# Performance work log

Hardware: AMD Instinct MI355X
Metric: run time of the kernel (lower is better)

## Reference

```python
import jax, jax.numpy as jnp
import numpy as np

N_NODES = 50000
N_EDGES = 500000
NFEAT = 128
NHID = 128
NOUT = 16


def setup_inputs() -> dict:
    key = jax.random.key(0)
    ks = jax.random.split(key, 8)
    x = jax.random.normal(ks[0], (N_NODES, NFEAT), dtype=jnp.float32)
    edge_src = jax.random.randint(ks[1], (N_EDGES,), 0, N_NODES, dtype=jnp.int32)
    edge_dst = jax.random.randint(ks[2], (N_EDGES,), 0, N_NODES, dtype=jnp.int32)
    edge_weight = jax.random.uniform(ks[3], (N_EDGES,), dtype=jnp.float32)
    # Glorot-ish init for linear weights, zero bias (PyG GCNConv default bias=0)
    def glorot(k, fan_in, fan_out):
        s = jnp.sqrt(6.0 / (fan_in + fan_out))
        return jax.random.uniform(k, (fan_in, fan_out), jnp.float32, -s, s)
    W1 = glorot(ks[4], NFEAT, NHID)
    W2 = glorot(ks[5], NHID, NHID)
    W3 = glorot(ks[6], NHID, NOUT)
    b1 = jnp.zeros((NHID,), jnp.float32)
    b2 = jnp.zeros((NHID,), jnp.float32)
    b3 = jnp.zeros((NOUT,), jnp.float32)
    return {"x": x, "edge_src": edge_src, "edge_dst": edge_dst,
            "edge_weight": edge_weight, "W1": W1, "b1": b1,
            "W2": W2, "b2": b2, "W3": W3, "b3": b3}


def gcn_conv(x, src, dst, ew, W, b):
    """PyG GCNConv: symmetric-normalized aggregation with self-loops (weight 1).

    out_i = sum_{(j->i)} d_i^{-1/2} w_ji d_j^{-1/2} (x_j W) + d_i^{-1} (x_i W) + b
    where d_i = 1 + sum of incoming edge weights.
    """
    n = x.shape[0]
    xw = x @ W                                            # [N, F_out]
    deg = jax.ops.segment_sum(ew, dst, num_segments=n) + 1.0  # self-loop weight 1
    dinv = jnp.where(deg > 0, jax.lax.rsqrt(deg), 0.0)    # d^{-1/2}
    norm = dinv[src] * ew * dinv[dst]                     # [E]
    agg = jax.ops.segment_sum(xw[src] * norm[:, None], dst, num_segments=n)
    self_loop = xw * (dinv * dinv)[:, None]               # d_i^{-1} * x_i W
    return agg + self_loop + b


def reference(x, edge_src, edge_dst, edge_weight, W1, b1, W2, b2, W3, b3):
    # Dropout layers are identity in eval mode.
    h = gcn_conv(x, edge_src, edge_dst, edge_weight, W1, b1)
    h = jax.nn.relu(h)
    h = gcn_conv(h, edge_src, edge_dst, edge_weight, W2, b2)
    h = jax.nn.relu(h)
    h = gcn_conv(h, edge_src, edge_dst, edge_weight, W3, b3)
    return jax.nn.log_softmax(h, axis=1)
```

## Files before the change

### kernel.cpp

```cpp
#include <hip/hip_runtime.h>
#include <math.h>

#define NN 50000
#define NE 500000
#define NF 128
#define NO 16
#define SCAN_B 1024
#define NB_SCAN 49
#define NPART 16
#define EB4 489
#define EB2 977

static_assert(NN < 65536, "src must fit u16");

typedef _Float16 f16x8 __attribute__((ext_vector_type(8)));
typedef _Float16 f16x4 __attribute__((ext_vector_type(4)));
typedef float f32x4 __attribute__((ext_vector_type(4)));

union HU { unsigned short u; _Float16 h; };

__device__ inline float rec_w(unsigned int rec) {
    HU cu; cu.u = (unsigned short)(rec >> 16);
    return (float)cu.h;
}


__global__ __launch_bounds__(256) void k_count_rank(const int* __restrict__ dst,
                                                    int* __restrict__ pcnt,
                                                    int* __restrict__ rank, int E,
                                                    const float* __restrict__ W1,
                                                    const float* __restrict__ W2,
                                                    _Float16* __restrict__ W1T,
                                                    _Float16* __restrict__ W2T) {
    int b = blockIdx.x;
    if (b < EB4 - 1) {
        int part = b & (NPART - 1);
        int e0 = b * 1024 + threadIdx.x;
        int d0 = dst[e0], d1 = dst[e0 + 256], d2 = dst[e0 + 512], d3 = dst[e0 + 768];
        int r0 = atomicAdd(&pcnt[part * NN + d0], 1);
        int r1 = atomicAdd(&pcnt[part * NN + d1], 1);
        int r2 = atomicAdd(&pcnt[part * NN + d2], 1);
        int r3 = atomicAdd(&pcnt[part * NN + d3], 1);
        rank[e0]       = r0;
        rank[e0 + 256] = r1;
        rank[e0 + 512] = r2;
        rank[e0 + 768] = r3;
    } else if (b == EB4 - 1) {
        int part = b & (NPART - 1);
#pragma unroll
        for (int k = 0; k < 4; ++k) {
            int e = b * 1024 + k * 256 + threadIdx.x;
            if (e < E) {
                int d = dst[e];
                rank[e] = atomicAdd(&pcnt[part * NN + d], 1);
            }
        }
    } else {
        int idx = (b - EB4) * 256 + threadIdx.x;
        int r = idx >> 7, c = idx & 127;
        W1T[(size_t)c * NF + r] = (_Float16)W1[idx];
        W2T[(size_t)c * NF + r] = (_Float16)W2[idx];
    }
}

__global__ void k_scan1f(int* __restrict__ pcnt, int* __restrict__ offs_p,
                         int* __restrict__ bsums, int* __restrict__ done) {
    __shared__ int sm[SCAN_B];
    __shared__ int isLast;
    int t = threadIdx.x;
    int i = blockIdx.x * SCAN_B + t;
    int c = 0;
    if (i < NN) {
        int run = 0;
#pragma unroll
        for (int p = 0; p < NPART; ++p) {
            int v = pcnt[p * NN + i];
            pcnt[p * NN + i] = run;
            run += v;
        }
        c = run;
    }
    sm[t] = c;
    __syncthreads();
    for (int off = 1; off < SCAN_B; off <<= 1) {
        int x = (t >= off) ? sm[t - off] : 0;
        __syncthreads();
        sm[t] += x;
        __syncthreads();
    }
    if (i < NN) offs_p[i] = sm[t] - c;
    if (t == SCAN_B - 1) {
        __hip_atomic_store(&bsums[blockIdx.x], sm[t], __ATOMIC_RELEASE,
                           __HIP_MEMORY_SCOPE_AGENT);
        int old = __hip_atomic_fetch_add(done, 1, __ATOMIC_ACQ_REL,
                                         __HIP_MEMORY_SCOPE_AGENT);
        isLast = (old == (int)gridDim.x - 1) ? 1 : 0;
    }
    __syncthreads();
    if (isLast && t < 64) {
        int v = (t < NB_SCAN) ? __hip_atomic_load(&bsums[t], __ATOMIC_ACQUIRE,
                                                  __HIP_MEMORY_SCOPE_AGENT) : 0;
        int orig = v;
#pragma unroll
        for (int off = 1; off < 64; off <<= 1) {
            int u = __shfl_up(v, off, 64);
            if (t >= off) v += u;
        }
        if (t < NB_SCAN)
            __hip_atomic_store(&bsums[t], v - orig, __ATOMIC_RELEASE,
                               __HIP_MEMORY_SCOPE_AGENT);
    }
}

__global__ __launch_bounds__(256) void k_scatter(const int* __restrict__ src,
                                                 const int* __restrict__ dst,
                                                 const float* __restrict__ ew,
                                                 const int* __restrict__ pcnt,
                                                 const int* __restrict__ rank,
                                                 const int* __restrict__ offs_p,
                                                 const int* __restrict__ bsums,
                                                 unsigned int* __restrict__ erec, int E) {
    int b = blockIdx.x;
#pragma unroll
    for (int k = 0; k < 2; ++k) {
        int e = b * 512 + k * 256 + threadIdx.x;
        if (e < E) {
            int part = (e >> 10) & (NPART - 1);
            int d = dst[e];
            int pos = offs_p[d] + bsums[d >> 10] + pcnt[part * NN + d] + rank[e];
            HU cu; cu.h = (_Float16)ew[e];
            erec[pos] = (unsigned int)src[e] | ((unsigned int)cu.u << 16);
        }
    }
}

__global__ __launch_bounds__(256) void k_dinv_csr(const unsigned int* __restrict__ erec,
                                                  const int* __restrict__ offs_p,
                                                  const int* __restrict__ bsums,
                                                  float* __restrict__ dinv) {
    int tid = threadIdx.x;
    int g = tid >> 4, li = tid & 15;
    int n = blockIdx.x * 16 + g;
    if (n >= NN) return;
    int s = offs_p[n] + bsums[n >> 10];
    int e = (n + 1 < NN) ? offs_p[n + 1] + bsums[(n + 1) >> 10] : NE;
    float d = 0.f;
    for (int j = s + li; j < e; j += 16) d += rec_w(erec[j]);
#pragma unroll
    for (int off = 8; off > 0; off >>= 1) d += __shfl_xor(d, off, 16);
    if (li == 0) dinv[n] = rsqrtf(1.0f + d);
}


__device__ inline f16x8 afrag_load(const float* X, int row, int k0) {
    const float4* p = (const float4*)(X + (size_t)row * NF + k0);
    float4 a = p[0], b = p[1];
    f16x8 r;
    r[0] = (_Float16)a.x; r[1] = (_Float16)a.y; r[2] = (_Float16)a.z; r[3] = (_Float16)a.w;
    r[4] = (_Float16)b.x; r[5] = (_Float16)b.y; r[6] = (_Float16)b.z; r[7] = (_Float16)b.w;
    return r;
}
__device__ inline f16x8 afrag_load(const _Float16* X, int row, int k0) {
    return *(const f16x8*)(X + (size_t)row * NF + k0);
}

template <typename TA>
__global__ __launch_bounds__(256) void k_gemm_mfma(const TA* __restrict__ X,
                                                   const _Float16* __restrict__ WT,
                                                   const float* __restrict__ dinv,
                                                   _Float16* __restrict__ Z, int M) {
    __shared__ _Float16 ls[4][16 * 136];
    const int tid  = threadIdx.x;
    const int w    = tid >> 6;
    const int lane = tid & 63;
    const int n16  = lane & 15;
    const int quad = lane >> 4;
    const int r0   = blockIdx.x * 64 + w * 16;

    int arow = r0 + n16; if (arow > M - 1) arow = M - 1;

    f32x4 acc[8];
#pragma unroll
    for (int c = 0; c < 8; ++c) acc[c] = (f32x4){0.f, 0.f, 0.f, 0.f};

#pragma unroll
    for (int kk = 0; kk < 4; ++kk) {
        int k0 = kk * 32 + quad * 8;
        f16x8 a = afrag_load(X, arow, k0);
#pragma unroll
        for (int c = 0; c < 8; ++c) {
            f16x8 b = *(const f16x8*)(WT + (size_t)(c * 16 + n16) * NF + k0);
            acc[c] = __builtin_amdgcn_mfma_f32_16x16x32_f16(a, b, acc[c], 0, 0, 0);
        }
    }

#pragma unroll
    for (int reg = 0; reg < 4; ++reg) {
        int lrow = quad * 4 + reg;
        int grow = r0 + lrow; if (grow > M - 1) grow = M - 1;
        float di = dinv[grow];
#pragma unroll
        for (int c = 0; c < 8; ++c)
            ls[w][lrow * 136 + c * 16 + n16] = (_Float16)(acc[c][reg] * di);
    }
    __syncthreads();
#pragma unroll
    for (int i = 0; i < 4; ++i) {
        int off16 = i * 64 + lane;
        int row = off16 >> 4;
        int col = off16 & 15;
        int grow = r0 + row;
        if (grow < M) {
            f16x8 v = *(const f16x8*)(&ls[w][row * 136 + col * 8]);
            *(f16x8*)(Z + (size_t)grow * NF + col * 8) = v;
        }
    }
}

__global__ __launch_bounds__(256) void k_agg128h(const _Float16* __restrict__ z,
                                                 const float* __restrict__ dinv,
                                                 const int* __restrict__ offs_p,
                                                 const int* __restrict__ bsums,
                                                 const unsigned int* __restrict__ erec,
                                                 const float* __restrict__ bias,
                                                 _Float16* __restrict__ hout, int relu) {
    const int tid  = threadIdx.x;
    const int lane = tid & 63;
    const int q    = lane >> 4;
    const int li   = lane & 15;
    int n = __builtin_amdgcn_readfirstlane(blockIdx.x * 4 + (tid >> 6));

    float acc[8];
#pragma unroll
    for (int j = 0; j < 8; ++j) acc[j] = 0.f;

    int s = offs_p[n] + bsums[n >> 10];
    int e = (n + 1 < NN) ? offs_p[n + 1] + bsums[(n + 1) >> 10] : NE;
    for (int base = s; base < e; base += 64) {
        int cnt = e - base; if (cnt > 64) cnt = 64;
        unsigned int rec = 0u;
        if (lane < cnt) rec = erec[base + lane];
        int   my_s = rec & 0xFFFF;
        float my_w = rec_w(rec);
        int cm1 = cnt - 1;
        for (int k = 0; k < cnt; k += 16) {
            int   sv[4];
            float wv[4];
            f16x8 v[4];
#pragma unroll
            for (int t = 0; t < 4; ++t) {
                int ei = k + 4 * t + q;
                int ec = ei < cm1 ? ei : cm1;
                sv[t] = __shfl(my_s, ec, 64);
                float wt = __shfl(my_w, ec, 64);
                wv[t] = (ei < cnt) ? wt : 0.0f;
            }
#pragma unroll
            for (int t = 0; t < 4; ++t)
                v[t] = *(const f16x8*)(z + ((size_t)sv[t] << 7) + li * 8);
#pragma unroll
            for (int t = 0; t < 4; ++t) {
#pragma unroll
                for (int j = 0; j < 8; ++j)
                    acc[j] = fmaf((float)v[t][j], wv[t], acc[j]);
            }
        }
    }
#pragma unroll
    for (int j = 0; j < 8; ++j) {
        acc[j] += __shfl_xor(acc[j], 32, 64);
        acc[j] += __shfl_xor(acc[j], 16, 64);
    }

    f16x8 sv8 = *(const f16x8*)(z + ((size_t)n << 7) + li * 8);
    float di = dinv[n];
    float4 bb0 = *(const float4*)(bias + li * 8);
    float4 bb1 = *(const float4*)(bias + li * 8 + 4);
    float r[8];
    r[0] = fmaf(di, (float)sv8[0] + acc[0], bb0.x);
    r[1] = fmaf(di, (float)sv8[1] + acc[1], bb0.y);
    r[2] = fmaf(di, (float)sv8[2] + acc[2], bb0.z);
    r[3] = fmaf(di, (float)sv8[3] + acc[3], bb0.w);
    r[4] = fmaf(di, (float)sv8[4] + acc[4], bb1.x);
    r[5] = fmaf(di, (float)sv8[5] + acc[5], bb1.y);
    r[6] = fmaf(di, (float)sv8[6] + acc[6], bb1.z);
    r[7] = fmaf(di, (float)sv8[7] + acc[7], bb1.w);
    if (relu) {
#pragma unroll
        for (int j = 0; j < 8; ++j) r[j] = fmaxf(r[j], 0.0f);
    }
    if (q == 0) {
        f16x8 o;
#pragma unroll
        for (int j = 0; j < 8; ++j) o[j] = (_Float16)r[j];
        __builtin_nontemporal_store(o, (f16x8*)(hout + ((size_t)n << 7) + li * 8));
    }
}

__global__ __launch_bounds__(256) void k_gemm16(const _Float16* __restrict__ H,
                                                const float* __restrict__ W3,
                                                const float* __restrict__ dinv,
                                                _Float16* __restrict__ Z3, int M) {
    __shared__ float Wl[NF * NO];
    __shared__ float Hs[16 * 132];
    int tid = threadIdx.x;
    for (int i = tid; i < NF * NO; i += 256) Wl[i] = W3[i];
    int n0 = blockIdx.x * 16;
    {
        int row = tid >> 4, h8 = tid & 15;
        int gr = n0 + row; if (gr > M - 1) gr = M - 1;
        f16x8 v = *(const f16x8*)(H + (size_t)gr * NF + h8 * 8);
        float4 f0 = {(float)v[0], (float)v[1], (float)v[2], (float)v[3]};
        float4 f1 = {(float)v[4], (float)v[5], (float)v[6], (float)v[7]};
        *(float4*)(&Hs[row * 132 + h8 * 8])     = f0;
        *(float4*)(&Hs[row * 132 + h8 * 8 + 4]) = f1;
    }
    __syncthreads();
    int ln = tid >> 4, c = tid & 15;
    float acc = 0.0f;
#pragma unroll 8
    for (int k = 0; k < NF; ++k) acc = fmaf(Hs[ln * 132 + k], Wl[k * NO + c], acc);
    int n = n0 + ln;
    if (n < M) Z3[(size_t)n * NO + c] = (_Float16)(acc * dinv[n]);
}

__global__ __launch_bounds__(256) void k_agg16_ls(const _Float16* __restrict__ z3,
                                                  const float* __restrict__ dinv,
                                                  const int* __restrict__ offs_p,
                                                  const int* __restrict__ bsums,
                                                  const unsigned int* __restrict__ erec,
                                                  const float* __restrict__ bias,
                                                  float* __restrict__ out) {
    int tid = threadIdx.x;
    int ln = tid >> 4, c = tid & 15;
    int n = blockIdx.x * 16 + ln;
    float acc = (float)z3[((size_t)n << 4) + c];
    int s = offs_p[n] + bsums[n >> 10];
    int e = (n + 1 < NN) ? offs_p[n + 1] + bsums[(n + 1) >> 10] : NE;
    for (int k = s; k < e; k += 16) {
        float vv[16], ww[16];
#pragma unroll
        for (int t = 0; t < 16; ++t) {
            int idx = k + t;
            int ic = idx < e ? idx : e - 1;
            unsigned int r = erec[ic];
            vv[t] = (float)z3[((size_t)(r & 0xFFFF) << 4) + c];
            ww[t] = (idx < e) ? rec_w(r) : 0.0f;
        }
#pragma unroll
        for (int t = 0; t < 16; ++t) acc = fmaf(vv[t], ww[t], acc);
    }
    acc = fmaf(dinv[n], acc, bias[c]);
    float m = acc;
#pragma unroll
    for (int off = 8; off > 0; off >>= 1) m = fmaxf(m, __shfl_xor(m, off, 16));
    float ex = expf(acc - m);
    float ss = ex;
#pragma unroll
    for (int off = 8; off > 0; off >>= 1) ss += __shfl_xor(ss, off, 16);
    out[(size_t)n * NO + c] = acc - m - logf(ss);
}


extern "C" void kernel_launch(void* const* d_in, const int* in_sizes, int n_in,
                              void* d_out, int out_size, void* d_ws, size_t ws_size,
                              hipStream_t stream) {
    const float* x   = (const float*)d_in[0];
    const int*   esrc= (const int*)  d_in[1];
    const int*   edst= (const int*)  d_in[2];
    const float* ew  = (const float*)d_in[3];
    const float* W1  = (const float*)d_in[4];
    const float* b1  = (const float*)d_in[5];
    const float* W2  = (const float*)d_in[6];
    const float* b2  = (const float*)d_in[7];
    const float* W3  = (const float*)d_in[8];
    const float* b3  = (const float*)d_in[9];
    float* out = (float*)d_out;

    char* p = (char*)d_ws;
    _Float16* z   = (_Float16*)p; p += (size_t)NN * NF * 2;
    _Float16* h   = (_Float16*)p; p += (size_t)NN * NF * 2;
    _Float16* z3  = (_Float16*)p; p += (size_t)NN * NO * 2;
    float* dinv   = (float*)p; p += (size_t)NN * 4;
    unsigned int* erec = (unsigned int*)p; p += (size_t)NE * 4;
    int*   rank   = (int*)p;   p += (size_t)NE * 4;
    int*   pcnt   = (int*)p;   p += (size_t)NPART * NN * 4;
    int*   done   = (int*)p;   p += 64;
    int*   offs_p = (int*)p;   p += (size_t)(NN + 1) * 4;
    int*   bsums  = (int*)p;   p += 256;
    _Float16* W1T = (_Float16*)p; p += (size_t)NF * NF * 2;
    _Float16* W2T = (_Float16*)p; p += (size_t)NF * NF * 2;

    hipMemsetAsync(pcnt, 0, (size_t)NPART * NN * 4 + 64, stream);

    k_count_rank<<<EB4 + 64, 256, 0, stream>>>(edst, pcnt, rank, NE, W1, W2, W1T, W2T);
    k_scan1f<<<NB_SCAN, SCAN_B, 0, stream>>>(pcnt, offs_p, bsums, done);
    k_scatter<<<EB2, 256, 0, stream>>>(esrc, edst, ew, pcnt, rank, offs_p, bsums, erec, NE);
    k_dinv_csr<<<(NN + 15) / 16, 256, 0, stream>>>(erec, offs_p, bsums, dinv);

    k_gemm_mfma<float><<<(NN + 63) / 64, 256, 0, stream>>>(x, W1T, dinv, z, NN);
    k_agg128h<<<NN / 4, 256, 0, stream>>>(z, dinv, offs_p, bsums, erec, b1, h, 1);
    k_gemm_mfma<_Float16><<<(NN + 63) / 64, 256, 0, stream>>>(h, W2T, dinv, z, NN);
    k_agg128h<<<NN / 4, 256, 0, stream>>>(z, dinv, offs_p, bsums, erec, b2, h, 1);
    k_gemm16<<<(NN + 15) / 16, 256, 0, stream>>>(h, W3, dinv, z3, NN);
    k_agg16_ls<<<NN / 16, 256, 0, stream>>>(z3, dinv, offs_p, bsums, erec, b3, out);
}
```

Measured before the change: 240.1 us.

## Fuse degree computation into first GEMM and rework final aggregation per wave

New measurement: 245.0 us. 1.02x slower.

```diff
diff --git a/kernel.cpp b/kernel.cpp
--- a/kernel.cpp
+++ b/kernel.cpp
@@ -15,6 +15,7 @@
 
 typedef _Float16 f16x8 __attribute__((ext_vector_type(8)));
 typedef _Float16 f16x4 __attribute__((ext_vector_type(4)));
+typedef _Float16 f16x2 __attribute__((ext_vector_type(2)));
 typedef float f32x4 __attribute__((ext_vector_type(4)));
 
 union HU { unsigned short u; _Float16 h; };
@@ -134,23 +135,6 @@
     }
 }
 
-__global__ __launch_bounds__(256) void k_dinv_csr(const unsigned int* __restrict__ erec,
-                                                  const int* __restrict__ offs_p,
-                                                  const int* __restrict__ bsums,
-                                                  float* __restrict__ dinv) {
-    int tid = threadIdx.x;
-    int g = tid >> 4, li = tid & 15;
-    int n = blockIdx.x * 16 + g;
-    if (n >= NN) return;
-    int s = offs_p[n] + bsums[n >> 10];
-    int e = (n + 1 < NN) ? offs_p[n + 1] + bsums[(n + 1) >> 10] : NE;
-    float d = 0.f;
-    for (int j = s + li; j < e; j += 16) d += rec_w(erec[j]);
-#pragma unroll
-    for (int off = 8; off > 0; off >>= 1) d += __shfl_xor(d, off, 16);
-    if (li == 0) dinv[n] = rsqrtf(1.0f + d);
-}
-
 
 __device__ inline f16x8 afrag_load(const float* X, int row, int k0) {
     const float4* p = (const float4*)(X + (size_t)row * NF + k0);
@@ -164,12 +148,17 @@
     return *(const f16x8*)(X + (size_t)row * NF + k0);
 }
 
-template <typename TA>
+template <typename TA, bool CDINV>
 __global__ __launch_bounds__(256) void k_gemm_mfma(const TA* __restrict__ X,
                                                    const _Float16* __restrict__ WT,
                                                    const float* __restrict__ dinv,
+                                                   float* __restrict__ dinv_out,
+                                                   const int* __restrict__ offs_p,
+                                                   const int* __restrict__ bsums,
+                                                   const unsigned int* __restrict__ erec,
                                                    _Float16* __restrict__ Z, int M) {
     __shared__ _Float16 ls[4][16 * 136];
+    __shared__ float ld[64];
     const int tid  = threadIdx.x;
     const int w    = tid >> 6;
     const int lane = tid & 63;
@@ -177,6 +166,29 @@
     const int quad = lane >> 4;
     const int r0   = blockIdx.x * 64 + w * 16;
 
+    if (CDINV) {
+        int j = tid >> 2, li = tid & 3;
+        int n = blockIdx.x * 64 + j;
+        int nc = n < M ? n : M - 1;
+        int s = offs_p[nc] + bsums[nc >> 10];
+        int e = (nc + 1 < NN) ? offs_p[nc + 1] + bsums[(nc + 1) >> 10] : NE;
+        float d = 0.f;
+        for (int t = s + li; t < e; t += 4) d += rec_w(erec[t]);
+        d += __shfl_xor(d, 1, 64);
+        d += __shfl_xor(d, 2, 64);
+        float di = rsqrtf(1.0f + d);
+        if (li == 0) {
+            ld[j] = di;
+            if (n < M) dinv_out[n] = di;
+        }
+    } else {
+        if (tid < 64) {
+            int n = blockIdx.x * 64 + tid;
+            ld[tid] = dinv[n < M ? n : M - 1];
+        }
+    }
+    __syncthreads();
+
     int arow = r0 + n16; if (arow > M - 1) arow = M - 1;
 
     f32x4 acc[8];
@@ -197,8 +209,7 @@
 #pragma unroll
     for (int reg = 0; reg < 4; ++reg) {
         int lrow = quad * 4 + reg;
-        int grow = r0 + lrow; if (grow > M - 1) grow = M - 1;
-        float di = dinv[grow];
+        float di = ld[w * 16 + lrow];
 #pragma unroll
         for (int c = 0; c < 8; ++c)
             ls[w][lrow * 136 + c * 16 + n16] = (_Float16)(acc[c][reg] * di);
@@ -331,34 +342,62 @@
                                                   const unsigned int* __restrict__ erec,
                                                   const float* __restrict__ bias,
                                                   float* __restrict__ out) {
-    int tid = threadIdx.x;
-    int ln = tid >> 4, c = tid & 15;
-    int n = blockIdx.x * 16 + ln;
-    float acc = (float)z3[((size_t)n << 4) + c];
+    const int tid  = threadIdx.x;
+    const int lane = tid & 63;
+    const int g    = lane >> 3;
+    const int f    = lane & 7;
+    int n = __builtin_amdgcn_readfirstlane(blockIdx.x * 4 + (tid >> 6));
+
+    float acc0 = 0.f, acc1 = 0.f;
     int s = offs_p[n] + bsums[n >> 10];
     int e = (n + 1 < NN) ? offs_p[n + 1] + bsums[(n + 1) >> 10] : NE;
-    for (int k = s; k < e; k += 16) {
-        float vv[16], ww[16];
-#pragma unroll
-        for (int t = 0; t < 16; ++t) {
-            int idx = k + t;
-            int ic = idx < e ? idx : e - 1;
-            unsigned int r = erec[ic];
-            vv[t] = (float)z3[((size_t)(r & 0xFFFF) << 4) + c];
-            ww[t] = (idx < e) ? rec_w(r) : 0.0f;
-        }
-#pragma unroll
-        for (int t = 0; t < 16; ++t) acc = fmaf(vv[t], ww[t], acc);
-    }
-    acc = fmaf(dinv[n], acc, bias[c]);
-    float m = acc;
-#pragma unroll
-    for (int off = 8; off > 0; off >>= 1) m = fmaxf(m, __shfl_xor(m, off, 16));
-    float ex = expf(acc - m);
-    float ss = ex;
-#pragma unroll
-    for (int off = 8; off > 0; off >>= 1) ss += __shfl_xor(ss, off, 16);
-    out[(size_t)n * NO + c] = acc - m - logf(ss);
+    for (int base = s; base < e; base += 64) {
+        int cnt = e - base; if (cnt > 64) cnt = 64;
+        unsigned int rec = 0u;
+        if (lane < cnt) rec = erec[base + lane];
+        int   my_s = rec & 0xFFFF;
+        float my_w = rec_w(rec);
+        int cm1 = cnt - 1;
+        for (int k = 0; k < cnt; k += 16) {
+            int ea = k + g, eb = k + 8 + g;
+            int ca = ea < cm1 ? ea : cm1;
+            int cb = eb < cm1 ? eb : cm1;
+            int sa = __shfl(my_s, ca, 64);
+            int sb = __shfl(my_s, cb, 64);
+            float wta = __shfl(my_w, ca, 64);
+            float wtb = __shfl(my_w, cb, 64);
+            float wa = (ea < cnt) ? wta : 0.0f;
+            float wb = (eb < cnt) ? wtb : 0.0f;
+            f16x2 va = *(const f16x2*)(z3 + ((size_t)sa << 4) + f * 2);
+            f16x2 vb = *(const f16x2*)(z3 + ((size_t)sb << 4) + f * 2);
+            acc0 = fmaf((float)va[0], wa, acc0);
+            acc1 = fmaf((float)va[1], wa, acc1);
+            acc0 = fmaf((float)vb[0], wb, acc0);
+            acc1 = fmaf((float)vb[1], wb, acc1);
+        }
+    }
+    acc0 += __shfl_xor(acc0, 8, 64);  acc1 += __shfl_xor(acc1, 8, 64);
+    acc0 += __shfl_xor(acc0, 16, 64); acc1 += __shfl_xor(acc1, 16, 64);
+    acc0 += __shfl_xor(acc0, 32, 64); acc1 += __shfl_xor(acc1, 32, 64);
+
+    f16x2 sv2 = *(const f16x2*)(z3 + ((size_t)n << 4) + f * 2);
+    float di = dinv[n];
+    float r0 = fmaf(di, (float)sv2[0] + acc0, bias[f * 2]);
+    float r1 = fmaf(di, (float)sv2[1] + acc1, bias[f * 2 + 1]);
+
+    float m = fmaxf(r0, r1);
+    m = fmaxf(m, __shfl_xor(m, 1, 64));
+    m = fmaxf(m, __shfl_xor(m, 2, 64));
+    m = fmaxf(m, __shfl_xor(m, 4, 64));
+    float ss = expf(r0 - m) + expf(r1 - m);
+    ss += __shfl_xor(ss, 1, 64);
+    ss += __shfl_xor(ss, 2, 64);
+    ss += __shfl_xor(ss, 4, 64);
+    float ls = logf(ss);
+    if (g == 0) {
+        float2 o = {r0 - m - ls, r1 - m - ls};
+        *(float2*)(out + (size_t)n * NO + f * 2) = o;
+    }
 }
 
 
@@ -396,12 +435,13 @@
     k_count_rank<<<EB4 + 64, 256, 0, stream>>>(edst, pcnt, rank, NE, W1, W2, W1T, W2T);
     k_scan1f<<<NB_SCAN, SCAN_B, 0, stream>>>(pcnt, offs_p, bsums, done);
     k_scatter<<<EB2, 256, 0, stream>>>(esrc, edst, ew, pcnt, rank, offs_p, bsums, erec, NE);
-    k_dinv_csr<<<(NN + 15) / 16, 256, 0, stream>>>(erec, offs_p, bsums, dinv);
-
-    k_gemm_mfma<float><<<(NN + 63) / 64, 256, 0, stream>>>(x, W1T, dinv, z, NN);
+
+    k_gemm_mfma<float, true><<<(NN + 63) / 64, 256, 0, stream>>>(
+        x, W1T, dinv, dinv, offs_p, bsums, erec, z, NN);
     k_agg128h<<<NN / 4, 256, 0, stream>>>(z, dinv, offs_p, bsums, erec, b1, h, 1);
-    k_gemm_mfma<_Float16><<<(NN + 63) / 64, 256, 0, stream>>>(h, W2T, dinv, z, NN);
+    k_gemm_mfma<_Float16, false><<<(NN + 63) / 64, 256, 0, stream>>>(
+        h, W2T, dinv, dinv, offs_p, bsums, erec, z, NN);
     k_agg128h<<<NN / 4, 256, 0, stream>>>(z, dinv, offs_p, bsums, erec, b2, h, 1);
     k_gemm16<<<(NN + 15) / 16, 256, 0, stream>>>(h, W3, dinv, z3, NN);
-    k_agg16_ls<<<NN / 16, 256, 0, stream>>>(z3, dinv, offs_p, bsums, erec, b3, out);
-}
+    k_agg16_ls<<<NN / 4, 256, 0, stream>>>(z3, dinv, offs_p, bsums, erec, b3, out);
+}
```

## Store hidden features in 16-wide column chunks and aggregate per chunk

Applied to the files above, without the earlier changes.

Result: slower. 277.5 us (+15.6%).

```diff
diff --git a/kernel.cpp b/kernel.cpp
--- a/kernel.cpp
+++ b/kernel.cpp
@@ -160,11 +160,11 @@
     r[4] = (_Float16)b.x; r[5] = (_Float16)b.y; r[6] = (_Float16)b.z; r[7] = (_Float16)b.w;
     return r;
 }
-__device__ inline f16x8 afrag_load(const _Float16* X, int row, int k0) {
-    return *(const f16x8*)(X + (size_t)row * NF + k0);
-}
-
-template <typename TA>
+__device__ inline f16x8 cfrag_load(const _Float16* Xc, int row, int k0) {
+    return *(const f16x8*)(Xc + ((size_t)(k0 >> 4) * NN + row) * 16 + (k0 & 15));
+}
+
+template <typename TA, bool CHUNKA>
 __global__ __launch_bounds__(256) void k_gemm_mfma(const TA* __restrict__ X,
                                                    const _Float16* __restrict__ WT,
                                                    const float* __restrict__ dinv,
@@ -186,7 +186,9 @@
 #pragma unroll
     for (int kk = 0; kk < 4; ++kk) {
         int k0 = kk * 32 + quad * 8;
-        f16x8 a = afrag_load(X, arow, k0);
+        f16x8 a;
+        if constexpr (CHUNKA) a = cfrag_load((const _Float16*)X, arow, k0);
+        else                  a = afrag_load(X, arow, k0);
 #pragma unroll
         for (int c = 0; c < 8; ++c) {
             f16x8 b = *(const f16x8*)(WT + (size_t)(c * 16 + n16) * NF + k0);
@@ -212,88 +214,75 @@
         int grow = r0 + row;
         if (grow < M) {
             f16x8 v = *(const f16x8*)(&ls[w][row * 136 + col * 8]);
-            *(f16x8*)(Z + (size_t)grow * NF + col * 8) = v;
-        }
-    }
-}
-
-__global__ __launch_bounds__(256) void k_agg128h(const _Float16* __restrict__ z,
+            *(f16x8*)(Z + ((size_t)(col >> 1) * NN + grow) * 16 + (col & 1) * 8) = v;
+        }
+    }
+}
+
+__global__ __launch_bounds__(256) void k_agg128c(const _Float16* __restrict__ zc,
                                                  const float* __restrict__ dinv,
                                                  const int* __restrict__ offs_p,
                                                  const int* __restrict__ bsums,
                                                  const unsigned int* __restrict__ erec,
                                                  const float* __restrict__ bias,
-                                                 _Float16* __restrict__ hout, int relu) {
+                                                 _Float16* __restrict__ hc, int relu) {
     const int tid  = threadIdx.x;
     const int lane = tid & 63;
     const int q    = lane >> 4;
-    const int li   = lane & 15;
-    int n = __builtin_amdgcn_readfirstlane(blockIdx.x * 4 + (tid >> 6));
-
-    float acc[8];
-#pragma unroll
-    for (int j = 0; j < 8; ++j) acc[j] = 0.f;
+    const int t    = lane & 15;
+    const int es   = t >> 2;
+    const int f    = t & 3;
+    const int c    = blockIdx.x & 7;
+    const int ng   = blockIdx.x >> 3;
+    const int n    = ng * 16 + (tid >> 6) * 4 + q;
+    const size_t cbase = (size_t)c * NN;
 
     int s = offs_p[n] + bsums[n >> 10];
     int e = (n + 1 < NN) ? offs_p[n + 1] + bsums[(n + 1) >> 10] : NE;
-    for (int base = s; base < e; base += 64) {
-        int cnt = e - base; if (cnt > 64) cnt = 64;
+
+    float acc0 = 0.f, acc1 = 0.f, acc2 = 0.f, acc3 = 0.f;
+    for (int base = s; base < e; base += 16) {
+        int cnt = e - base; if (cnt > 16) cnt = 16;
         unsigned int rec = 0u;
-        if (lane < cnt) rec = erec[base + lane];
+        if (t < cnt) rec = erec[base + t];
         int   my_s = rec & 0xFFFF;
         float my_w = rec_w(rec);
         int cm1 = cnt - 1;
-        for (int k = 0; k < cnt; k += 16) {
-            int   sv[4];
-            float wv[4];
-            f16x8 v[4];
-#pragma unroll
-            for (int t = 0; t < 4; ++t) {
-                int ei = k + 4 * t + q;
-                int ec = ei < cm1 ? ei : cm1;
-                sv[t] = __shfl(my_s, ec, 64);
-                float wt = __shfl(my_w, ec, 64);
-                wv[t] = (ei < cnt) ? wt : 0.0f;
-            }
-#pragma unroll
-            for (int t = 0; t < 4; ++t)
-                v[t] = *(const f16x8*)(z + ((size_t)sv[t] << 7) + li * 8);
-#pragma unroll
-            for (int t = 0; t < 4; ++t) {
-#pragma unroll
-                for (int j = 0; j < 8; ++j)
-                    acc[j] = fmaf((float)v[t][j], wv[t], acc[j]);
-            }
-        }
-    }
-#pragma unroll
-    for (int j = 0; j < 8; ++j) {
-        acc[j] += __shfl_xor(acc[j], 32, 64);
-        acc[j] += __shfl_xor(acc[j], 16, 64);
-    }
-
-    f16x8 sv8 = *(const f16x8*)(z + ((size_t)n << 7) + li * 8);
-    float di = dinv[n];
-    float4 bb0 = *(const float4*)(bias + li * 8);
-    float4 bb1 = *(const float4*)(bias + li * 8 + 4);
-    float r[8];
-    r[0] = fmaf(di, (float)sv8[0] + acc[0], bb0.x);
-    r[1] = fmaf(di, (float)sv8[1] + acc[1], bb0.y);
-    r[2] = fmaf(di, (float)sv8[2] + acc[2], bb0.z);
-    r[3] = fmaf(di, (float)sv8[3] + acc[3], bb0.w);
-    r[4] = fmaf(di, (float)sv8[4] + acc[4], bb1.x);
-    r[5] = fmaf(di, (float)sv8[5] + acc[5], bb1.y);
-    r[6] = fmaf(di, (float)sv8[6] + acc[6], bb1.z);
-    r[7] = fmaf(di, (float)sv8[7] + acc[7], bb1.w);
-    if (relu) {
-#pragma unroll
-        for (int j = 0; j < 8; ++j) r[j] = fmaxf(r[j], 0.0f);
-    }
-    if (q == 0) {
-        f16x8 o;
-#pragma unroll
-        for (int j = 0; j < 8; ++j) o[j] = (_Float16)r[j];
-        __builtin_nontemporal_store(o, (f16x8*)(hout + ((size_t)n << 7) + li * 8));
+        for (int k = 0; k < cnt; k += 4) {
+            int ei = k + es;
+            int ec = ei < cm1 ? ei : cm1;
+            int sl = q * 16 + ec;
+            int   sv = __shfl(my_s, sl, 64);
+            float wt = __shfl(my_w, sl, 64);
+            float w  = (ei < cnt) ? wt : 0.0f;
+            f16x4 v = *(const f16x4*)(zc + (cbase + sv) * 16 + f * 4);
+            acc0 = fmaf((float)v[0], w, acc0);
+            acc1 = fmaf((float)v[1], w, acc1);
+            acc2 = fmaf((float)v[2], w, acc2);
+            acc3 = fmaf((float)v[3], w, acc3);
+        }
+    }
+    acc0 += __shfl_xor(acc0, 4, 64); acc0 += __shfl_xor(acc0, 8, 64);
+    acc1 += __shfl_xor(acc1, 4, 64); acc1 += __shfl_xor(acc1, 8, 64);
+    acc2 += __shfl_xor(acc2, 4, 64); acc2 += __shfl_xor(acc2, 8, 64);
+    acc3 += __shfl_xor(acc3, 4, 64); acc3 += __shfl_xor(acc3, 8, 64);
+
+    if (es == 0) {
+        f16x4 sv4 = *(const f16x4*)(zc + (cbase + n) * 16 + f * 4);
+        float di = dinv[n];
+        float4 bb = *(const float4*)(bias + c * 16 + f * 4);
+        float r0 = fmaf(di, (float)sv4[0] + acc0, bb.x);
+        float r1 = fmaf(di, (float)sv4[1] + acc1, bb.y);
+        float r2 = fmaf(di, (float)sv4[2] + acc2, bb.z);
+        float r3 = fmaf(di, (float)sv4[3] + acc3, bb.w);
+        if (relu) {
+            r0 = fmaxf(r0, 0.0f); r1 = fmaxf(r1, 0.0f);
+            r2 = fmaxf(r2, 0.0f); r3 = fmaxf(r3, 0.0f);
+        }
+        f16x4 o;
+        o[0] = (_Float16)r0; o[1] = (_Float16)r1;
+        o[2] = (_Float16)r2; o[3] = (_Float16)r3;
+        *(f16x4*)(hc + (cbase + n) * 16 + f * 4) = o;
     }
 }
 
@@ -309,7 +298,7 @@
     {
         int row = tid >> 4, h8 = tid & 15;
         int gr = n0 + row; if (gr > M - 1) gr = M - 1;
-        f16x8 v = *(const f16x8*)(H + (size_t)gr * NF + h8 * 8);
+        f16x8 v = *(const f16x8*)(H + ((size_t)(h8 >> 1) * NN + gr) * 16 + (h8 & 1) * 8);
         float4 f0 = {(float)v[0], (float)v[1], (float)v[2], (float)v[3]};
         float4 f1 = {(float)v[4], (float)v[5], (float)v[6], (float)v[7]};
         *(float4*)(&Hs[row * 132 + h8 * 8])     = f0;
@@ -391,17 +380,17 @@
     _Float16* W1T = (_Float16*)p; p += (size_t)NF * NF * 2;
     _Float16* W2T = (_Float16*)p; p += (size_t)NF * NF * 2;
 
-    hipMemsetAsync(pcnt, 0, (size_t)NPART * NN * 4 + 64, stream);
+    (void)hipMemsetAsync(pcnt, 0, (size_t)NPART * NN * 4 + 64, stream);
 
     k_count_rank<<<EB4 + 64, 256, 0, stream>>>(edst, pcnt, rank, NE, W1, W2, W1T, W2T);
     k_scan1f<<<NB_SCAN, SCAN_B, 0, stream>>>(pcnt, offs_p, bsums, done);
     k_scatter<<<EB2, 256, 0, stream>>>(esrc, edst, ew, pcnt, rank, offs_p, bsums, erec, NE);
     k_dinv_csr<<<(NN + 15) / 16, 256, 0, stream>>>(erec, offs_p, bsums, dinv);
 
-    k_gemm_mfma<float><<<(NN + 63) / 64, 256, 0, stream>>>(x, W1T, dinv, z, NN);
-    k_agg128h<<<NN / 4, 256, 0, stream>>>(z, dinv, offs_p, bsums, erec, b1, h, 1);
-    k_gemm_mfma<_Float16><<<(NN + 63) / 64, 256, 0, stream>>>(h, W2T, dinv, z, NN);
-    k_agg128h<<<NN / 4, 256, 0, stream>>>(z, dinv, offs_p, bsums, erec, b2, h, 1);
+    k_gemm_mfma<float, false><<<(NN + 63) / 64, 256, 0, stream>>>(x, W1T, dinv, z, NN);
+    k_agg128c<<<(NN / 16) * 8, 256, 0, stream>>>(z, dinv, offs_p, bsums, erec, b1, h, 1);
+    k_gemm_mfma<_Float16, true><<<(NN + 63) / 64, 256, 0, stream>>>(h, W2T, dinv, z, NN);
+    k_agg128c<<<(NN / 16) * 8, 256, 0, stream>>>(z, dinv, offs_p, bsums, erec, b2, h, 1);
     k_gemm16<<<(NN + 15) / 16, 256, 0, stream>>>(h, W3, dinv, z3, NN);
     k_agg16_ls<<<NN / 16, 256, 0, stream>>>(z3, dinv, offs_p, bsums, erec, b3, out);
 }
```

## Store GEMM output feature-chunked and aggregate per 32-feature chunk

Applied to the files above, without the earlier changes.

Measured after the change: 267.2 us. +11.3%, slower.

```diff
diff --git a/kernel.cpp b/kernel.cpp
--- a/kernel.cpp
+++ b/kernel.cpp
@@ -5,6 +5,7 @@
 #define NE 500000
 #define NF 128
 #define NO 16
+#define NCH 4
 #define SCAN_B 1024
 #define NB_SCAN 49
 #define NPART 16
@@ -212,12 +213,12 @@
         int grow = r0 + row;
         if (grow < M) {
             f16x8 v = *(const f16x8*)(&ls[w][row * 136 + col * 8]);
-            *(f16x8*)(Z + (size_t)grow * NF + col * 8) = v;
-        }
-    }
-}
-
-__global__ __launch_bounds__(256) void k_agg128h(const _Float16* __restrict__ z,
+            *(f16x8*)(Z + ((size_t)(col >> 2) * NN + grow) * 32 + (col & 3) * 8) = v;
+        }
+    }
+}
+
+__global__ __launch_bounds__(256) void k_agg128c(const _Float16* __restrict__ zc,
                                                  const float* __restrict__ dinv,
                                                  const int* __restrict__ offs_p,
                                                  const int* __restrict__ bsums,
@@ -227,73 +228,69 @@
     const int tid  = threadIdx.x;
     const int lane = tid & 63;
     const int q    = lane >> 4;
-    const int li   = lane & 15;
-    int n = __builtin_amdgcn_readfirstlane(blockIdx.x * 4 + (tid >> 6));
-
-    float acc[8];
-#pragma unroll
-    for (int j = 0; j < 8; ++j) acc[j] = 0.f;
+    const int t    = lane & 15;
+    const int es   = t >> 2;
+    const int f    = t & 3;
+    const int c    = blockIdx.x & 3;
+    const int ng   = blockIdx.x >> 2;
+    const int n    = ng * 16 + (tid >> 6) * 4 + q;
+    const size_t cbase = (size_t)c * NN;
 
     int s = offs_p[n] + bsums[n >> 10];
     int e = (n + 1 < NN) ? offs_p[n + 1] + bsums[(n + 1) >> 10] : NE;
-    for (int base = s; base < e; base += 64) {
-        int cnt = e - base; if (cnt > 64) cnt = 64;
+
+    float acc[8];
+#pragma unroll
+    for (int j = 0; j < 8; ++j) acc[j] = 0.f;
+
+    for (int base = s; base < e; base += 16) {
+        int cnt = e - base; if (cnt > 16) cnt = 16;
         unsigned int rec = 0u;
-        if (lane < cnt) rec = erec[base + lane];
+        if (t < cnt) rec = __builtin_nontemporal_load(erec + base + t);
         int   my_s = rec & 0xFFFF;
         float my_w = rec_w(rec);
         int cm1 = cnt - 1;
-        for (int k = 0; k < cnt; k += 16) {
-            int   sv[4];
-            float wv[4];
-            f16x8 v[4];
-#pragma unroll
-            for (int t = 0; t < 4; ++t) {
-                int ei = k + 4 * t + q;
-                int ec = ei < cm1 ? ei : cm1;
-                sv[t] = __shfl(my_s, ec, 64);
-                float wt = __shfl(my_w, ec, 64);
-                wv[t] = (ei < cnt) ? wt : 0.0f;
-            }
-#pragma unroll
-            for (int t = 0; t < 4; ++t)
-                v[t] = *(const f16x8*)(z + ((size_t)sv[t] << 7) + li * 8);
-#pragma unroll
-            for (int t = 0; t < 4; ++t) {
-#pragma unroll
-                for (int j = 0; j < 8; ++j)
-                    acc[j] = fmaf((float)v[t][j], wv[t], acc[j]);
-            }
+        for (int k = 0; k < cnt; k += 4) {
+            int ei = k + es;
+            int ec = ei < cm1 ? ei : cm1;
+            int sl = q * 16 + ec;
+            int   sv = __shfl(my_s, sl, 64);
+            float wt = __shfl(my_w, sl, 64);
+            float w  = (ei < cnt) ? wt : 0.0f;
+            f16x8 v = *(const f16x8*)(zc + (cbase + sv) * 32 + f * 8);
+#pragma unroll
+            for (int j = 0; j < 8; ++j)
+                acc[j] = fmaf((float)v[j], w, acc[j]);
         }
     }
 #pragma unroll
     for (int j = 0; j < 8; ++j) {
-        acc[j] += __shfl_xor(acc[j], 32, 64);
-        acc[j] += __shfl_xor(acc[j], 16, 64);
-    }
-
-    f16x8 sv8 = *(const f16x8*)(z + ((size_t)n << 7) + li * 8);
-    float di = dinv[n];
-    float4 bb0 = *(const float4*)(bias + li * 8);
-    float4 bb1 = *(const float4*)(bias + li * 8 + 4);
-    float r[8];
-    r[0] = fmaf(di, (float)sv8[0] + acc[0], bb0.x);
-    r[1] = fmaf(di, (float)sv8[1] + acc[1], bb0.y);
-    r[2] = fmaf(di, (float)sv8[2] + acc[2], bb0.z);
-    r[3] = fmaf(di, (float)sv8[3] + acc[3], bb0.w);
-    r[4] = fmaf(di, (float)sv8[4] + acc[4], bb1.x);
-    r[5] = fmaf(di, (float)sv8[5] + acc[5], bb1.y);
-    r[6] = fmaf(di, (float)sv8[6] + acc[6], bb1.z);
-    r[7] = fmaf(di, (float)sv8[7] + acc[7], bb1.w);
-    if (relu) {
-#pragma unroll
-        for (int j = 0; j < 8; ++j) r[j] = fmaxf(r[j], 0.0f);
-    }
-    if (q == 0) {
+        acc[j] += __shfl_xor(acc[j], 4, 64);
+        acc[j] += __shfl_xor(acc[j], 8, 64);
+    }
+
+    if (es == 0) {
+        f16x8 sv8 = *(const f16x8*)(zc + (cbase + n) * 32 + f * 8);
+        float di = dinv[n];
+        float4 bb0 = *(const float4*)(bias + c * 32 + f * 8);
+        float4 bb1 = *(const float4*)(bias + c * 32 + f * 8 + 4);
+        float r[8];
+        r[0] = fmaf(di, (float)sv8[0] + acc[0], bb0.x);
+        r[1] = fmaf(di, (float)sv8[1] + acc[1], bb0.y);
+        r[2] = fmaf(di, (float)sv8[2] + acc[2], bb0.z);
+        r[3] = fmaf(di, (float)sv8[3] + acc[3], bb0.w);
+        r[4] = fmaf(di, (float)sv8[4] + acc[4], bb1.x);
+        r[5] = fmaf(di, (float)sv8[5] + acc[5], bb1.y);
+        r[6] = fmaf(di, (float)sv8[6] + acc[6], bb1.z);
+        r[7] = fmaf(di, (float)sv8[7] + acc[7], bb1.w);
+        if (relu) {
+#pragma unroll
+            for (int j = 0; j < 8; ++j) r[j] = fmaxf(r[j], 0.0f);
+        }
         f16x8 o;
 #pragma unroll
         for (int j = 0; j < 8; ++j) o[j] = (_Float16)r[j];
-        __builtin_nontemporal_store(o, (f16x8*)(hout + ((size_t)n << 7) + li * 8));
+        *(f16x8*)(hout + (size_t)n * NF + c * 32 + f * 8) = o;
     }
 }
 
@@ -391,7 +388,7 @@
     _Float16* W1T = (_Float16*)p; p += (size_t)NF * NF * 2;
     _Float16* W2T = (_Float16*)p; p += (size_t)NF * NF * 2;
 
-    hipMemsetAsync(pcnt, 0, (size_t)NPART * NN * 4 + 64, stream);
+    (void)hipMemsetAsync(pcnt, 0, (size_t)NPART * NN * 4 + 64, stream);
 
     k_count_rank<<<EB4 + 64, 256, 0, stream>>>(edst, pcnt, rank, NE, W1, W2, W1T, W2T);
     k_scan1f<<<NB_SCAN, SCAN_B, 0, stream>>>(pcnt, offs_p, bsums, done);
@@ -399,9 +396,9 @@
     k_dinv_csr<<<(NN + 15) / 16, 256, 0, stream>>>(erec, offs_p, bsums, dinv);
 
     k_gemm_mfma<float><<<(NN + 63) / 64, 256, 0, stream>>>(x, W1T, dinv, z, NN);
-    k_agg128h<<<NN / 4, 256, 0, stream>>>(z, dinv, offs_p, bsums, erec, b1, h, 1);
+    k_agg128c<<<(NN / 16) * NCH, 256, 0, stream>>>(z, dinv, offs_p, bsums, erec, b1, h, 1);
     k_gemm_mfma<_Float16><<<(NN + 63) / 64, 256, 0, stream>>>(h, W2T, dinv, z, NN);
-    k_agg128h<<<NN / 4, 256, 0, stream>>>(z, dinv, offs_p, bsums, erec, b2, h, 1);
+    k_agg128c<<<(NN / 16) * NCH, 256, 0, stream>>>(z, dinv, offs_p, bsums, erec, b2, h, 1);
     k_gemm16<<<(NN + 15) / 16, 256, 0, stream>>>(h, W3, dinv, z3, NN);
     k_agg16_ls<<<NN / 16, 256, 0, stream>>>(z3, dinv, offs_p, bsums, erec, b3, out);
 }
```
